# Optimization experiments

Hardware: AMD Instinct MI355X
Metric: run time of the kernel (lower is better)

Reference implementation:

```python
import jax, jax.numpy as jnp
import numpy as np

D_MODEL, N_HEADS, D_VALUE = 512, 8, 64
D_HEAD = D_MODEL // N_HEADS


def setup_inputs() -> dict:
    key = jax.random.key(0)
    ks = jax.random.split(key, 5)
    B, T = 2, 2048
    x = jax.random.normal(ks[0], (B, T, D_MODEL), dtype=jnp.float32)
    # torch nn.Linear convention: W has shape [out_features, in_features]
    scale = 0.02
    W_q = jax.random.normal(ks[1], (N_HEADS * D_HEAD, D_MODEL), dtype=jnp.float32) * scale
    W_k = jax.random.normal(ks[2], (N_HEADS * D_HEAD, D_MODEL), dtype=jnp.float32) * scale
    W_v = jax.random.normal(ks[3], (N_HEADS * D_VALUE, D_MODEL), dtype=jnp.float32) * scale
    W_out = jax.random.normal(ks[4], (D_MODEL, N_HEADS * D_VALUE), dtype=jnp.float32) * scale
    return {"x": x, "W_q": W_q, "W_k": W_k, "W_v": W_v, "W_out": W_out}


def _elu_feature_map(t):
    # phi(t) = elu(t) + 1
    return jax.nn.elu(t) + 1.0


def reference(x, W_q, W_k, W_v, W_out):
    B, T, D = x.shape
    H, dh, dv = N_HEADS, D_HEAD, D_VALUE
    # projections (Linear without bias: x @ W.T)
    Q = _elu_feature_map((x @ W_q.T).reshape(B, T, H, dh)).transpose(0, 2, 1, 3)  # [B,H,T,dh]
    K = _elu_feature_map((x @ W_k.T).reshape(B, T, H, dh)).transpose(0, 2, 1, 3)  # [B,H,T,dh]
    V = (x @ W_v.T).reshape(B, T, H, dv).transpose(0, 2, 1, 3)                    # [B,H,T,dv]
    # causal linear attention via cumulative outer-product state
    KV = jnp.einsum('bhti,bhtj->bhtij', K, V)       # [B,H,T,dh,dv]
    S = jnp.cumsum(KV, axis=2)                      # running state
    z = jnp.cumsum(K, axis=2)                       # running normalizer
    num = jnp.einsum('bhti,bhtij->bhtj', Q, S)      # [B,H,T,dv]
    den = jnp.maximum(jnp.einsum('bhti,bhti->bht', Q, z), 1e-6)[..., None]
    out = (num / den).transpose(0, 2, 1, 3).reshape(B, T, H * dv)
    return out @ W_out.T
```

## Files before the change

### kernel.cpp

```cpp
#include <hip/hip_runtime.h>
#include <hip/hip_bf16.h>

#define T_SEQ 2048
#define BATCH 2
#define DMODEL 512
#define NHEAD 8
#define DHEAD 64
#define DVAL 64
#define BH 16
#define CHUNK 64
#define NCHUNK 32
#define MROWS 4096

typedef __bf16 bf16;
typedef __bf16 bf16x8 __attribute__((ext_vector_type(8)));
typedef __bf16 bf16x4 __attribute__((ext_vector_type(4)));
typedef float f32x4 __attribute__((ext_vector_type(4)));

__device__ inline void gload_lds16(const bf16* g, bf16* l) {
  __builtin_amdgcn_global_load_lds((const __attribute__((address_space(1))) void*)g,
                                   (__attribute__((address_space(3))) void*)l, 16, 0, 0);
}

__device__ inline int sw_t(int row, int g) {
  return ((g ^ (row & 7) ^ (row >> 3)) << 3);
}

__global__ void k_convert(const float* __restrict__ x,
                          const float* __restrict__ wq,
                          const float* __restrict__ wk,
                          const float* __restrict__ wv,
                          const float* __restrict__ wo,
                          bf16* __restrict__ x_bf,
                          bf16* __restrict__ wqkv_bf,
                          bf16* __restrict__ wo_bf) {
  const int W = DMODEL * DMODEL;
  int stride = gridDim.x * blockDim.x;
  int i0 = blockIdx.x * blockDim.x + threadIdx.x;
  for (int i = i0; i < MROWS * DMODEL; i += stride) x_bf[i] = (bf16)x[i];
  for (int i = i0; i < W; i += stride) {
    wqkv_bf[i]         = (bf16)wq[i];
    wqkv_bf[W + i]     = (bf16)wk[i];
    wqkv_bf[2 * W + i] = (bf16)wv[i];
    wo_bf[i]           = (bf16)wo[i];
  }
}

template <int EPI>
__global__ __launch_bounds__(256) void k_gemm(const bf16* __restrict__ A,
                                              const bf16* __restrict__ B,
                                              bf16* __restrict__ Q,
                                              bf16* __restrict__ K,
                                              bf16* __restrict__ V,
                                              float* __restrict__ out) {
  __shared__ bf16 As[128 * 32];
  __shared__ bf16 Bs[128 * 32];
  const int tid = threadIdx.x;
  const int wv = tid >> 6, lane = tid & 63;
  const int c = lane & 15, quad = lane >> 4;
  const int m_tile = blockIdx.x * 128, n_tile = blockIdx.y * 128;
  const int lrow = lane >> 2, lcol = (lane & 3) * 8;
  const bf16* Abase = A + (size_t)m_tile * DMODEL;
  const bf16* Bbase = B + (size_t)n_tile * DMODEL;
  const int wm = (wv >> 1) * 64, wn = (wv & 1) * 64;

  f32x4 acc[4][4] = {};

  for (int k0 = 0; k0 < DMODEL; k0 += 32) {
    if (k0) __syncthreads();
#pragma unroll
    for (int r = 0; r < 2; r++) {
      int t = wv + r * 4;
      const bf16* ga = Abase + (size_t)(t * 16 + lrow) * DMODEL + k0 + lcol;
      const bf16* gb = Bbase + (size_t)(t * 16 + lrow) * DMODEL + k0 + lcol;
      gload_lds16(ga, As + t * 16 * 32);
      gload_lds16(gb, Bs + t * 16 * 32);
    }
    __syncthreads();
    bf16x8 af[4], bfr[4];
#pragma unroll
    for (int i = 0; i < 4; i++)
      af[i] = *(const bf16x8*)(As + (wm + i * 16 + c) * 32 + quad * 8);
#pragma unroll
    for (int j = 0; j < 4; j++)
      bfr[j] = *(const bf16x8*)(Bs + (wn + j * 16 + c) * 32 + quad * 8);
#pragma unroll
    for (int i = 0; i < 4; i++)
#pragma unroll
      for (int j = 0; j < 4; j++)
        acc[i][j] = __builtin_amdgcn_mfma_f32_16x16x32_bf16(af[i], bfr[j], acc[i][j], 0, 0, 0);
  }

#pragma unroll
  for (int i = 0; i < 4; i++) {
#pragma unroll
    for (int j = 0; j < 4; j++) {
      int n = n_tile + wn + j * 16 + c;
#pragma unroll
      for (int r = 0; r < 4; r++) {
        int m = m_tile + wm + i * 16 + quad * 4 + r;
        float v = acc[i][j][r];
        if (EPI == 0) {
          if (n < 1024) v = (v > 0.f) ? (v + 1.f) : __expf(v);
          bf16 o = (bf16)v;
          if (n < 512)       Q[(size_t)m * 512 + n] = o;
          else if (n < 1024) K[(size_t)m * 512 + (n - 512)] = o;
          else               V[(size_t)m * 512 + (n - 1024)] = o;
        } else {
          out[(size_t)m * DMODEL + n] = v;
        }
      }
    }
  }
}

__global__ __launch_bounds__(256) void k_state(const bf16* __restrict__ K,
                                               const bf16* __restrict__ V,
                                               float* __restrict__ KVs,
                                               float* __restrict__ zsum) {
  __shared__ bf16 Kt[4096];
  __shared__ bf16 Vt[4096];
  int chunk = blockIdx.x, bh = blockIdx.y;
  int b = bh >> 3, h = bh & 7;
  int tid = threadIdx.x, lane = tid & 63, wv = tid >> 6;
  int rowbase = b * T_SEQ + chunk * CHUNK;

#pragma unroll
  for (int p = 0; p < 2; p++) {
    int r = p * 32 + (tid >> 3);
    int j0 = (tid & 7) * 8;
    bf16x8 kk = *(const bf16x8*)(K + (size_t)(rowbase + r) * 512 + h * 64 + j0);
    bf16x8 vvv = *(const bf16x8*)(V + (size_t)(rowbase + r) * 512 + h * 64 + j0);
#pragma unroll
    for (int u = 0; u < 8; u++) {
      int row = j0 + u;
      Kt[row * 64 + sw_t(row, r >> 3) + (r & 7)] = kk[u];
      Vt[row * 64 + sw_t(row, r >> 3) + (r & 7)] = vvv[u];
    }
  }
  __syncthreads();

  int c = lane & 15, quad = lane >> 4;
  f32x4 acc[4] = {};
#pragma unroll
  for (int ks = 0; ks < 2; ks++) {
    int ar = wv * 16 + c;
    bf16x8 a = *(const bf16x8*)(Vt + ar * 64 + sw_t(ar, ks * 4 + quad));
#pragma unroll
    for (int f = 0; f < 4; f++) {
      int br = f * 16 + c;
      bf16x8 bb = *(const bf16x8*)(Kt + br * 64 + sw_t(br, ks * 4 + quad));
      acc[f] = __builtin_amdgcn_mfma_f32_16x16x32_bf16(a, bb, acc[f], 0, 0, 0);
    }
  }
  float* op = KVs + ((size_t)(bh * NCHUNK + chunk) << 12);
#pragma unroll
  for (int f = 0; f < 4; f++)
#pragma unroll
    for (int r = 0; r < 4; r++)
      op[(wv * 16 + quad * 4 + r) * 64 + f * 16 + c] = acc[f][r];

  if (tid < 64) {
    float s = 0.f;
#pragma unroll
    for (int g = 0; g < 8; g++) {
      bf16x8 kr = *(const bf16x8*)(Kt + tid * 64 + sw_t(tid, g));
#pragma unroll
      for (int u = 0; u < 8; u++) s += (float)kr[u];
    }
    zsum[(size_t)(bh * NCHUNK + chunk) * 64 + tid] = s;
  }
}

__global__ __launch_bounds__(256) void k_attn(const bf16* __restrict__ Q,
                                              const bf16* __restrict__ K,
                                              const bf16* __restrict__ V,
                                              const float* __restrict__ KVs,
                                              const float* __restrict__ zsum,
                                              bf16* __restrict__ O) {
  __shared__ bf16 Qs[4096];
  __shared__ bf16 Ks[4096];
  __shared__ bf16 Vt[4096];
  __shared__ bf16 As[4096];
  __shared__ bf16 Spre[4096];
  __shared__ float zp4[4][64];
  __shared__ float zpre[64], rsum[64], den[64];

  int chunk = blockIdx.x, bh = blockIdx.y;
  int b = bh >> 3, h = bh & 7;
  int tid = threadIdx.x, lane = tid & 63, wv = tid >> 6;
  int c = lane & 15, quad = lane >> 4;
  int rowbase = b * T_SEQ + chunk * CHUNK;

#pragma unroll
  for (int p = 0; p < 2; p++) {
    int rbase = p * 32 + wv * 8;
    int r8 = lane >> 3, gp = lane & 7;
    const bf16* gq = Q + (size_t)(rowbase + rbase + r8) * 512 + h * 64 + ((gp ^ r8) << 3);
    const bf16* gk = K + (size_t)(rowbase + rbase + r8) * 512 + h * 64 + ((gp ^ r8) << 3);
    gload_lds16(gq, Qs + rbase * 64);
    gload_lds16(gk, Ks + rbase * 64);
  }

#pragma unroll
  for (int p = 0; p < 2; p++) {
    int r = p * 32 + (tid >> 3);
    int j0 = (tid & 7) * 8;
    bf16x8 vvv = *(const bf16x8*)(V + (size_t)(rowbase + r) * 512 + h * 64 + j0);
#pragma unroll
    for (int u = 0; u < 8; u++) {
      int row = j0 + u;
      Vt[row * 64 + sw_t(row, r >> 3) + (r & 7)] = vvv[u];
    }
  }

  {
    float accp[16];
#pragma unroll
    for (int u = 0; u < 16; u++) accp[u] = 0.f;
    const float* base = KVs + ((size_t)(bh * NCHUNK) << 12) + tid * 16;
    for (int cc = 0; cc < chunk; cc++) {
      const float* pp = base + ((size_t)cc << 12);
#pragma unroll
      for (int q4 = 0; q4 < 4; q4++) {
        f32x4 v4 = *(const f32x4*)(pp + q4 * 4);
#pragma unroll
        for (int u = 0; u < 4; u++) accp[q4 * 4 + u] += v4[u];
      }
    }
    int j = tid >> 2, i0 = (tid & 3) * 16;
#pragma unroll
    for (int u = 0; u < 16; u++) {
      int i = i0 + u;
      Spre[j * 64 + sw_t(j, i >> 3) + (i & 7)] = (bf16)accp[u];
    }
  }

  {
    int i = tid & 63, qq = tid >> 6;
    float s = 0.f;
    for (int cc = qq; cc < chunk; cc += 4)
      s += zsum[(size_t)(bh * NCHUNK + cc) * 64 + i];
    zp4[qq][i] = s;
  }
  __syncthreads();
  if (tid < 64) zpre[tid] = zp4[0][tid] + zp4[1][tid] + zp4[2][tid] + zp4[3][tid];

  f32x4 sacc[4] = {};
#pragma unroll
  for (int ks = 0; ks < 2; ks++) {
    int ar = 16 * wv + c;
    bf16x8 a = *(const bf16x8*)(Qs + ar * 64 + (((ks * 4 + quad) ^ (c & 7)) << 3));
#pragma unroll
    for (int j = 0; j < 4; j++) {
      int br = 16 * j + c;
      bf16x8 bb = *(const bf16x8*)(Ks + br * 64 + (((ks * 4 + quad) ^ (c & 7)) << 3));
      sacc[j] = __builtin_amdgcn_mfma_f32_16x16x32_bf16(a, bb, sacc[j], 0, 0, 0);
    }
  }

  float rs[4] = {0.f, 0.f, 0.f, 0.f};
#pragma unroll
  for (int j = 0; j < 4; j++) {
#pragma unroll
    for (int r = 0; r < 4; r++) {
      int t = 16 * wv + quad * 4 + r, s = 16 * j + c;
      float v = (s <= t) ? sacc[j][r] : 0.f;
      rs[r] += v;
      As[t * 64 + sw_t(t, s >> 3) + (s & 7)] = (bf16)v;
    }
  }
#pragma unroll
  for (int r = 0; r < 4; r++) {
    float v = rs[r];
    v += __shfl_xor(v, 1); v += __shfl_xor(v, 2);
    v += __shfl_xor(v, 4); v += __shfl_xor(v, 8);
    if (c == 0) rsum[16 * wv + quad * 4 + r] = v;
  }
  __syncthreads();

  if (tid < 64) {
    float s = rsum[tid];
    int t7 = tid & 7;
#pragma unroll
    for (int kg = 0; kg < 8; kg++) {
      bf16x8 qv = *(const bf16x8*)(Qs + tid * 64 + ((kg ^ t7) << 3));
#pragma unroll
      for (int u = 0; u < 8; u++) s += (float)qv[u] * zpre[kg * 8 + u];
    }
    den[tid] = fmaxf(s, 1e-6f);
  }

  f32x4 oacc[4] = {};
#pragma unroll
  for (int ks = 0; ks < 2; ks++) {
    int ar = 16 * wv + c;
    bf16x8 aq = *(const bf16x8*)(Qs + ar * 64 + (((ks * 4 + quad) ^ (c & 7)) << 3));
    bf16x8 aa = *(const bf16x8*)(As + ar * 64 + sw_t(ar, ks * 4 + quad));
#pragma unroll
    for (int j = 0; j < 4; j++) {
      int br = 16 * j + c;
      bf16x8 bs = *(const bf16x8*)(Spre + br * 64 + sw_t(br, ks * 4 + quad));
      bf16x8 bv = *(const bf16x8*)(Vt + br * 64 + sw_t(br, ks * 4 + quad));
      oacc[j] = __builtin_amdgcn_mfma_f32_16x16x32_bf16(aq, bs, oacc[j], 0, 0, 0);
      oacc[j] = __builtin_amdgcn_mfma_f32_16x16x32_bf16(aa, bv, oacc[j], 0, 0, 0);
    }
  }
  __syncthreads();
#pragma unroll
  for (int r = 0; r < 4; r++) {
    int t = 16 * wv + quad * 4 + r;
    float rd = 1.f / den[t];
#pragma unroll
    for (int j = 0; j < 4; j++)
      O[(size_t)(rowbase + t) * 512 + h * 64 + 16 * j + c] = (bf16)(oacc[j][r] * rd);
  }
}

extern "C" void kernel_launch(void* const* d_in, const int* in_sizes, int n_in,
                              void* d_out, int out_size, void* d_ws, size_t ws_size,
                              hipStream_t stream) {
  const float* x  = (const float*)d_in[0];
  const float* wq = (const float*)d_in[1];
  const float* wk = (const float*)d_in[2];
  const float* wv = (const float*)d_in[3];
  const float* wo = (const float*)d_in[4];
  float* out = (float*)d_out;

  char* p = (char*)d_ws;
  bf16* x_bf   = (bf16*)p; p += (size_t)MROWS * DMODEL * 2;
  bf16* wqkv_b = (bf16*)p; p += (size_t)3 * DMODEL * DMODEL * 2;
  bf16* wo_b   = (bf16*)p; p += (size_t)DMODEL * DMODEL * 2;
  bf16* Qb     = (bf16*)p; p += (size_t)MROWS * 512 * 2;
  bf16* Kb     = (bf16*)p; p += (size_t)MROWS * 512 * 2;
  bf16* Vb     = (bf16*)p; p += (size_t)MROWS * 512 * 2;
  bf16* Ob     = (bf16*)p; p += (size_t)MROWS * 512 * 2;
  float* KVs   = (float*)p; p += (size_t)BH * NCHUNK * DHEAD * DVAL * 4;
  float* zs    = (float*)p; p += (size_t)BH * NCHUNK * DHEAD * 4;

  k_convert<<<2048, 256, 0, stream>>>(x, wq, wk, wv, wo, x_bf, wqkv_b, wo_b);
  k_gemm<0><<<dim3(MROWS / 128, (3 * DMODEL) / 128), 256, 0, stream>>>(
      x_bf, wqkv_b, Qb, Kb, Vb, nullptr);
  k_state<<<dim3(NCHUNK, BH), 256, 0, stream>>>(Kb, Vb, KVs, zs);
  k_attn<<<dim3(NCHUNK, BH), 256, 0, stream>>>(Qb, Kb, Vb, KVs, zs, Ob);
  k_gemm<1><<<dim3(MROWS / 128, DMODEL / 128), 256, 0, stream>>>(
      Ob, wo_b, nullptr, nullptr, nullptr, out);
}
```

Baseline: 125.2 us.

## Vectorize conversion, deepen GEMM K-tile with swizzled LDS, store chunk states in bf16

The fp32-to-bf16 conversion kernel now converts four elements per thread with one vector load and store instead of a grid-stride scalar loop. The GEMM stages a K-slice of 64 instead of 32 per barrier, with an XOR-swizzled LDS layout to avoid bank conflicts, which halves the number of sync rounds. Per-chunk KV states are written and read back as bf16 instead of fp32, halving the traffic of the prefix-sum in the attention kernel. The cost is lower precision in the accumulated chunk states.

```diff
diff --git a/kernel.cpp b/kernel.cpp
--- a/kernel.cpp
+++ b/kernel.cpp
@@ -26,7 +26,7 @@
   return ((g ^ (row & 7) ^ (row >> 3)) << 3);
 }
 
-__global__ void k_convert(const float* __restrict__ x,
+__global__ __launch_bounds__(256) void k_convert(const float* __restrict__ x,
                           const float* __restrict__ wq,
                           const float* __restrict__ wk,
                           const float* __restrict__ wv,
@@ -35,14 +35,24 @@
                           bf16* __restrict__ wqkv_bf,
                           bf16* __restrict__ wo_bf) {
   const int W = DMODEL * DMODEL;
-  int stride = gridDim.x * blockDim.x;
-  int i0 = blockIdx.x * blockDim.x + threadIdx.x;
-  for (int i = i0; i < MROWS * DMODEL; i += stride) x_bf[i] = (bf16)x[i];
-  for (int i = i0; i < W; i += stride) {
-    wqkv_bf[i]         = (bf16)wq[i];
-    wqkv_bf[W + i]     = (bf16)wk[i];
-    wqkv_bf[2 * W + i] = (bf16)wv[i];
-    wo_bf[i]           = (bf16)wo[i];
+  int i = blockIdx.x * 256 + threadIdx.x;
+  {
+    f32x4 v = ((const f32x4*)x)[i];
+    bf16x4 o; o[0] = (bf16)v[0]; o[1] = (bf16)v[1]; o[2] = (bf16)v[2]; o[3] = (bf16)v[3];
+    *(bf16x4*)(x_bf + (size_t)i * 4) = o;
+  }
+  if (i < W / 4) {
+    f32x4 a = ((const f32x4*)wq)[i];
+    f32x4 b = ((const f32x4*)wk)[i];
+    f32x4 c = ((const f32x4*)wv)[i];
+    f32x4 d = ((const f32x4*)wo)[i];
+    bf16x4 oa, ob, oc, od;
+#pragma unroll
+    for (int u = 0; u < 4; u++) { oa[u] = (bf16)a[u]; ob[u] = (bf16)b[u]; oc[u] = (bf16)c[u]; od[u] = (bf16)d[u]; }
+    *(bf16x4*)(wqkv_bf + (size_t)i * 4) = oa;
+    *(bf16x4*)(wqkv_bf + W + (size_t)i * 4) = ob;
+    *(bf16x4*)(wqkv_bf + 2 * W + (size_t)i * 4) = oc;
+    *(bf16x4*)(wo_bf + (size_t)i * 4) = od;
   }
 }
 
@@ -53,42 +63,45 @@
                                               bf16* __restrict__ K,
                                               bf16* __restrict__ V,
                                               float* __restrict__ out) {
-  __shared__ bf16 As[128 * 32];
-  __shared__ bf16 Bs[128 * 32];
+  __shared__ bf16 As[128 * 64];
+  __shared__ bf16 Bs[128 * 64];
   const int tid = threadIdx.x;
   const int wv = tid >> 6, lane = tid & 63;
   const int c = lane & 15, quad = lane >> 4;
   const int m_tile = blockIdx.x * 128, n_tile = blockIdx.y * 128;
-  const int lrow = lane >> 2, lcol = (lane & 3) * 8;
+  const int r8 = lane >> 3, gp = lane & 7;
   const bf16* Abase = A + (size_t)m_tile * DMODEL;
   const bf16* Bbase = B + (size_t)n_tile * DMODEL;
   const int wm = (wv >> 1) * 64, wn = (wv & 1) * 64;
 
   f32x4 acc[4][4] = {};
 
-  for (int k0 = 0; k0 < DMODEL; k0 += 32) {
+  for (int k0 = 0; k0 < DMODEL; k0 += 64) {
     if (k0) __syncthreads();
 #pragma unroll
-    for (int r = 0; r < 2; r++) {
-      int t = wv + r * 4;
-      const bf16* ga = Abase + (size_t)(t * 16 + lrow) * DMODEL + k0 + lcol;
-      const bf16* gb = Bbase + (size_t)(t * 16 + lrow) * DMODEL + k0 + lcol;
-      gload_lds16(ga, As + t * 16 * 32);
-      gload_lds16(gb, Bs + t * 16 * 32);
+    for (int r = 0; r < 4; r++) {
+      int t = wv * 4 + r;
+      const bf16* ga = Abase + (size_t)(t * 8 + r8) * DMODEL + k0 + ((gp ^ r8) << 3);
+      const bf16* gb = Bbase + (size_t)(t * 8 + r8) * DMODEL + k0 + ((gp ^ r8) << 3);
+      gload_lds16(ga, As + t * 8 * 64);
+      gload_lds16(gb, Bs + t * 8 * 64);
     }
     __syncthreads();
-    bf16x8 af[4], bfr[4];
-#pragma unroll
-    for (int i = 0; i < 4; i++)
-      af[i] = *(const bf16x8*)(As + (wm + i * 16 + c) * 32 + quad * 8);
-#pragma unroll
-    for (int j = 0; j < 4; j++)
-      bfr[j] = *(const bf16x8*)(Bs + (wn + j * 16 + c) * 32 + quad * 8);
-#pragma unroll
-    for (int i = 0; i < 4; i++)
+#pragma unroll
+    for (int ks = 0; ks < 2; ks++) {
+      bf16x8 af[4], bfr[4];
+#pragma unroll
+      for (int i = 0; i < 4; i++)
+        af[i] = *(const bf16x8*)(As + (wm + i * 16 + c) * 64 + (((ks * 4 + quad) ^ (c & 7)) << 3));
 #pragma unroll
       for (int j = 0; j < 4; j++)
-        acc[i][j] = __builtin_amdgcn_mfma_f32_16x16x32_bf16(af[i], bfr[j], acc[i][j], 0, 0, 0);
+        bfr[j] = *(const bf16x8*)(Bs + (wn + j * 16 + c) * 64 + (((ks * 4 + quad) ^ (c & 7)) << 3));
+#pragma unroll
+      for (int i = 0; i < 4; i++)
+#pragma unroll
+        for (int j = 0; j < 4; j++)
+          acc[i][j] = __builtin_amdgcn_mfma_f32_16x16x32_bf16(af[i], bfr[j], acc[i][j], 0, 0, 0);
+    }
   }
 
 #pragma unroll
@@ -116,7 +129,7 @@
 
 __global__ __launch_bounds__(256) void k_state(const bf16* __restrict__ K,
                                                const bf16* __restrict__ V,
-                                               float* __restrict__ KVs,
+                                               bf16* __restrict__ KVs,
                                                float* __restrict__ zsum) {
   __shared__ bf16 Kt[4096];
   __shared__ bf16 Vt[4096];
@@ -153,12 +166,12 @@
       acc[f] = __builtin_amdgcn_mfma_f32_16x16x32_bf16(a, bb, acc[f], 0, 0, 0);
     }
   }
-  float* op = KVs + ((size_t)(bh * NCHUNK + chunk) << 12);
+  bf16* op = KVs + ((size_t)(bh * NCHUNK + chunk) << 12);
 #pragma unroll
   for (int f = 0; f < 4; f++)
 #pragma unroll
     for (int r = 0; r < 4; r++)
-      op[(wv * 16 + quad * 4 + r) * 64 + f * 16 + c] = acc[f][r];
+      op[(wv * 16 + quad * 4 + r) * 64 + f * 16 + c] = (bf16)acc[f][r];
 
   if (tid < 64) {
     float s = 0.f;
@@ -175,7 +188,7 @@
 __global__ __launch_bounds__(256) void k_attn(const bf16* __restrict__ Q,
                                               const bf16* __restrict__ K,
                                               const bf16* __restrict__ V,
-                                              const float* __restrict__ KVs,
+                                              const bf16* __restrict__ KVs,
                                               const float* __restrict__ zsum,
                                               bf16* __restrict__ O) {
   __shared__ bf16 Qs[4096];
@@ -218,15 +231,13 @@
     float accp[16];
 #pragma unroll
     for (int u = 0; u < 16; u++) accp[u] = 0.f;
-    const float* base = KVs + ((size_t)(bh * NCHUNK) << 12) + tid * 16;
+    const bf16* base = KVs + ((size_t)(bh * NCHUNK) << 12) + tid * 16;
     for (int cc = 0; cc < chunk; cc++) {
-      const float* pp = base + ((size_t)cc << 12);
-#pragma unroll
-      for (int q4 = 0; q4 < 4; q4++) {
-        f32x4 v4 = *(const f32x4*)(pp + q4 * 4);
-#pragma unroll
-        for (int u = 0; u < 4; u++) accp[q4 * 4 + u] += v4[u];
-      }
+      const bf16* pp = base + ((size_t)cc << 12);
+      bf16x8 a0 = *(const bf16x8*)pp;
+      bf16x8 a1 = *(const bf16x8*)(pp + 8);
+#pragma unroll
+      for (int u = 0; u < 8; u++) { accp[u] += (float)a0[u]; accp[8 + u] += (float)a1[u]; }
     }
     int j = tid >> 2, i0 = (tid & 3) * 16;
 #pragma unroll
@@ -335,7 +346,7 @@
   bf16* Kb     = (bf16*)p; p += (size_t)MROWS * 512 * 2;
   bf16* Vb     = (bf16*)p; p += (size_t)MROWS * 512 * 2;
   bf16* Ob     = (bf16*)p; p += (size_t)MROWS * 512 * 2;
-  float* KVs   = (float*)p; p += (size_t)BH * NCHUNK * DHEAD * DVAL * 4;
+  bf16* KVs    = (bf16*)p; p += (size_t)BH * NCHUNK * DHEAD * DVAL * 2;
   float* zs    = (float*)p; p += (size_t)BH * NCHUNK * DHEAD * 4;
 
   k_convert<<<2048, 256, 0, stream>>>(x, wq, wk, wv, wo, x_bf, wqkv_b, wo_b);
```

Result: faster. 119.9 us (-4.3%).
